# Performance work log

Hardware: AMD Instinct MI355X
Metric: run time of the kernel (lower is better)

Reference implementation:

```python
import jax, jax.numpy as jnp
import numpy as np

LEAKY_SLOPE = 0.01  # torch nn.LeakyReLU default
SOFTMAX_SCALE = 10.0
RATIO = 4


def _conv(x, w, b, stride, pad=1):
    y = jax.lax.conv_general_dilated(
        x, w, window_strides=(stride, stride), padding=[(pad, pad), (pad, pad)],
        dimension_numbers=("NCHW", "OIHW", "NCHW"))
    return y + b[None, :, None, None]


def _lrelu(x):
    return jnp.where(x >= 0, x, LEAKY_SLOPE * x)


def setup_inputs() -> dict:
    key = jax.random.key(0)
    ks = jax.random.split(key, 11)
    band_ms, band_hs = 8, 128
    inp = {
        "hrms": jax.random.normal(ks[0], (2, band_ms, 512, 512), jnp.float32),
        "msi": jax.random.normal(ks[1], (2, band_ms, 512, 512), jnp.float32),
        "hsi": jax.random.normal(ks[2], (2, band_hs, 128, 128), jnp.float32),
        "Wv": jax.random.normal(ks[3], (band_ms, band_ms, 3, 3), jnp.float32) * 0.05,
        "bv": jax.random.normal(ks[4], (band_ms,), jnp.float32) * 0.05,
        "Wq": jax.random.normal(ks[5], (band_ms, band_ms, 3, 3), jnp.float32) * 0.05,
        "bq": jax.random.normal(ks[6], (band_ms,), jnp.float32) * 0.05,
        "Wk": jax.random.normal(ks[7], (band_hs, band_hs, 3, 3), jnp.float32) * 0.05,
        "bk": jax.random.normal(ks[8], (band_hs,), jnp.float32) * 0.05,
        "Wr": jax.random.normal(ks[9], (band_hs, band_hs, 3, 3), jnp.float32) * 0.05,
        "br": jax.random.normal(ks[10], (band_hs,), jnp.float32) * 0.05,
    }
    return inp


def reference(hrms, msi, hsi, Wv, bv, Wq, bq, Wk, bk, Wr, br):
    # conv_v: 3x3 stride 1; conv_q: 3x3 stride ratio**2; conv_k: 3x3 stride ratio
    v = _lrelu(_conv(hrms, Wv, bv, 1))                 # (N, band_ms, H, W)
    q = _lrelu(_conv(msi, Wq, bq, RATIO * RATIO))      # (N, band_ms, 32, 32)
    k = _lrelu(_conv(hsi, Wk, bk, RATIO))              # (N, band_hs, 32, 32)

    # per-sample scalar normalization: max over bands of ||q_band||_2
    k0_max = jnp.max(jnp.sqrt(jnp.sum(q * q, axis=(2, 3))), axis=1)  # (N,)
    qn = q / k0_max[:, None, None, None]

    # Conv_spe with full-extent filter and stride == filter size reduces to a
    # global cross-spectral correlation: att[n, i, c] = <k[n,c], qn[n,i]>
    att = jnp.einsum("nihw,nchw->nic", qn, k)          # (N, band_ms, band_hs)
    att = jax.nn.softmax(att * SOFTMAX_SCALE, axis=2)  # softmax over band_hs

    # conv_transpose2d with 1x1 kernel (band_ms, band_hs, 1, 1) = pointwise mix
    out = jnp.einsum("nihw,nic->nchw", v, att) / 6.0   # (N, band_hs, H, W)
    return _lrelu(_conv(out, Wr, br, 1))
```

## Files before the change

### kernel.cpp

```cpp
#include <hip/hip_runtime.h>
#include <hip/hip_bf16.h>

#define LK 0.01f
__device__ __forceinline__ float lrelu(float x){ return x >= 0.f ? x : LK * x; }

#define NB 2
#define CMS 8
#define CHS 128
#define HW 512
#define HSIN 128
#define OS 32
#define K72 72

#define OFF_V   0
#define SZ_V    (NB*CMS*HW*HW)
#define OFF_Q   (OFF_V + SZ_V)
#define SZ_Q    (NB*CMS*OS*OS)
#define OFF_K   (OFF_Q + SZ_Q)
#define SZ_K    (NB*CHS*OS*OS)
#define OFF_BN  (OFF_K + SZ_K)
#define OFF_AR  (OFF_BN + 64)
#define SZ_AR   (NB*CMS*CHS)
#define OFF_A2  (OFF_AR + SZ_AR)
#define OFF_WE  (OFF_A2 + SZ_AR)
#define SZ_WE   (NB*K72*CHS)
#define OFF_WKT (OFF_WE + SZ_WE)
#define SZ_WKT  (1152*CHS)
#define OFF_WVT (OFF_WKT + SZ_WKT)
#define SZ_WVT  (K72*CMS)

__global__ void prep_kernel(const float* __restrict__ Wk, const float* __restrict__ Wv,
                            float* __restrict__ wkt, float* __restrict__ wvT){
  int idx = blockIdx.x * 256 + threadIdx.x;
  if (idx < 147456){
    int co = idx & 127, kk = idx >> 7;
    wkt[kk*128 + co] = Wk[co*1152 + kk];
  } else if (idx < 147456 + 576){
    int l = idx - 147456;
    int co = l & 7, kt = l >> 3;
    wvT[kt*8 + co] = Wv[co*72 + kt];
  }
}

__global__ __launch_bounds__(256, 4)
void conv_v_kernel(const float* __restrict__ hrms, const float* __restrict__ wvT,
                   const float* __restrict__ bv, float* __restrict__ v){
  __shared__ float vt[CMS][34][36];
  __shared__ __align__(16) float wl[K72*CMS];
  __shared__ float bvs[CMS];
  int xt = blockIdx.x, yt = blockIdx.y, n = blockIdx.z;
  int tid = threadIdx.x;
  for (int l = tid; l < CMS*34*34; l += 256){
    int ci = l / 1156, r = l % 1156, yy = r / 34, xx = r % 34;
    int gy = yt*32 + yy - 1, gx = xt*32 + xx - 1;
    float val = 0.f;
    if ((unsigned)gy < HW && (unsigned)gx < HW)
      val = hrms[((n*CMS+ci)*HW + gy)*HW + gx];
    vt[ci][yy][xx] = val;
  }
  for (int l = tid; l < K72*CMS; l += 256) wl[l] = wvT[l];
  if (tid < CMS) bvs[tid] = bv[tid];
  __syncthreads();
  int wid = tid >> 6;
  int lane = tid & 63;
  int lrow = lane >> 5, lx = lane & 31;
  for (int s = wid; s < 16; s += 4){
    int r0 = s*2 + lrow;
    float acc[8];
    #pragma unroll
    for (int c = 0; c < 8; c++) acc[c] = 0.f;
    #pragma unroll
    for (int ci = 0; ci < 8; ci++){
      float vv[9];
      #pragma unroll
      for (int t = 0; t < 9; t++) vv[t] = vt[ci][r0 + t/3][lx + t%3];
      #pragma unroll
      for (int tap = 0; tap < 9; tap++){
        const float4* wp = (const float4*)&wl[(ci*9 + tap)*8];
        float4 w0 = wp[0], w1 = wp[1];
        float vvt = vv[tap];
        acc[0] += w0.x*vvt; acc[1] += w0.y*vvt; acc[2] += w0.z*vvt; acc[3] += w0.w*vvt;
        acc[4] += w1.x*vvt; acc[5] += w1.y*vvt; acc[6] += w1.z*vvt; acc[7] += w1.w*vvt;
      }
    }
    int gy = yt*32 + r0, gx = xt*32 + lx;
    #pragma unroll
    for (int c = 0; c < 8; c++)
      v[((n*CMS+c)*HW + gy)*HW + gx] = lrelu(acc[c] + bvs[c]);
  }
}

__global__ void conv_q_kernel(const float* __restrict__ msi, const float* __restrict__ Wq,
                              const float* __restrict__ bq, float* __restrict__ q){
  __shared__ float rows[CMS][3][512];
  __shared__ float wq[K72*CMS];
  __shared__ float bqs[CMS];
  int n = blockIdx.x >> 5, y = blockIdx.x & 31;
  int tid = threadIdx.x;
  int y0 = y*16 - 1;
  for (int l = tid; l < CMS*3*512; l += 256){
    int ci = l / 1536, r = l % 1536, rr = r >> 9, xx = r & 511;
    int gy = y0 + rr;
    float val = 0.f;
    if ((unsigned)gy < HW) val = msi[((n*CMS+ci)*HW + gy)*HW + xx];
    rows[ci][rr][xx] = val;
  }
  for (int l = tid; l < K72*CMS; l += 256) wq[l] = Wq[l];
  if (tid < CMS) bqs[tid] = bq[tid];
  __syncthreads();
  int x = tid & 31, co = tid >> 5;
  int x0 = x*16 - 1;
  float acc = bqs[co];
  #pragma unroll
  for (int ci = 0; ci < 8; ci++){
    #pragma unroll
    for (int tap = 0; tap < 9; tap++){
      int xi = x0 + tap%3;
      float vv = ((unsigned)xi < HW) ? rows[ci][tap/3][xi] : 0.f;
      acc += vv * wq[co*72 + ci*9 + tap];
    }
  }
  q[((n*CMS+co)*OS + y)*OS + x] = lrelu(acc);
}

__global__ void bandnorm_kernel(const float* __restrict__ q, float* __restrict__ bn){
  int b = blockIdx.x;
  int tid = threadIdx.x;
  const float* qb = q + b*1024;
  float s = 0.f;
  for (int j = tid; j < 1024; j += 256){ float v = qb[j]; s += v*v; }
  __shared__ float red[4];
  for (int off = 32; off; off >>= 1) s += __shfl_down(s, off);
  if ((tid & 63) == 0) red[tid >> 6] = s;
  __syncthreads();
  if (tid == 0) bn[b] = sqrtf(red[0] + red[1] + red[2] + red[3]);
}

__global__ void conv_k_kernel(const float* __restrict__ hsi, const float* __restrict__ wkt,
                              const float* __restrict__ bk, float* __restrict__ kw){
  __shared__ __align__(16) float patch[1152][4];
  int xg = blockIdx.x, y = blockIdx.y, n = blockIdx.z;
  int tid = threadIdx.x;
  for (int l = tid; l < 4608; l += 128){
    int kk = l >> 2, xi = l & 3;
    int ci = kk / 9, tap = kk % 9;
    int gy = 4*y + tap/3 - 1, gx = 4*(xg*4 + xi) + tap%3 - 1;
    float val = 0.f;
    if ((unsigned)gy < HSIN && (unsigned)gx < HSIN)
      val = hsi[((n*CHS+ci)*HSIN + gy)*HSIN + gx];
    patch[kk][xi] = val;
  }
  __syncthreads();
  int co = tid;
  float bkv = bk[co];
  float a0 = bkv, a1 = bkv, a2 = bkv, a3 = bkv;
  #pragma unroll 8
  for (int kk = 0; kk < 1152; kk++){
    float4 p = *(const float4*)patch[kk];
    float w = wkt[kk*128 + co];
    a0 += p.x * w; a1 += p.y * w; a2 += p.z * w; a3 += p.w * w;
  }
  int base = ((n*CHS + co)*OS + y)*OS + xg*4;
  kw[base + 0] = lrelu(a0); kw[base + 1] = lrelu(a1);
  kw[base + 2] = lrelu(a2); kw[base + 3] = lrelu(a3);
}

__global__ void att_kernel(const float* __restrict__ q, const float* __restrict__ kw,
                           const float* __restrict__ bn, float* __restrict__ ar){
  int n = blockIdx.x >> 7, c = blockIdx.x & 127;
  int tid = threadIdx.x;
  const float* kb = kw + (n*CHS + c)*1024;
  float kreg[8];
  #pragma unroll
  for (int u = 0; u < 8; u++) kreg[u] = kb[tid + u*128];
  float m = bn[n*8];
  #pragma unroll
  for (int i = 1; i < 8; i++) m = fmaxf(m, bn[n*8 + i]);
  __shared__ float red[2];
  for (int i = 0; i < 8; i++){
    const float* qb = q + (n*CMS + i)*1024;
    float s = 0.f;
    #pragma unroll
    for (int u = 0; u < 8; u++) s += qb[tid + u*128] * kreg[u];
    for (int off = 32; off; off >>= 1) s += __shfl_down(s, off);
    if ((tid & 63) == 0) red[tid >> 6] = s;
    __syncthreads();
    if (tid == 0) ar[(n*CMS + i)*CHS + c] = (red[0] + red[1]) / m;
    __syncthreads();
  }
}

__global__ void softmax_kernel(const float* __restrict__ ar, float* __restrict__ a2){
  int b = blockIdx.x;
  int tid = threadIdx.x;
  float x = ar[b*128 + tid] * 10.f;
  __shared__ float red[2];
  float m = x;
  for (int off = 32; off; off >>= 1) m = fmaxf(m, __shfl_xor(m, off));
  if ((tid & 63) == 0) red[tid >> 6] = m;
  __syncthreads();
  m = fmaxf(red[0], red[1]);
  float e = expf(x - m);
  float s = e;
  for (int off = 32; off; off >>= 1) s += __shfl_xor(s, off);
  __syncthreads();
  if ((tid & 63) == 0) red[tid >> 6] = s;
  __syncthreads();
  s = red[0] + red[1];
  a2[b*128 + tid] = e / (6.f * s);
}

__global__ void weff_kernel(const float* __restrict__ Wr, const float* __restrict__ a2,
                            float* __restrict__ weT){
  int o = blockIdx.x & 127, n = blockIdx.x >> 7;
  int t = threadIdx.x;
  if (t >= 72) return;
  int i = t / 9, tap = t % 9;
  const float* av = a2 + (n*CMS + i)*CHS;
  float s = 0.f;
  for (int c = 0; c < 128; c++)
    s += Wr[(o*128 + c)*9 + tap] * av[c];
  weT[(n*K72 + t)*CHS + o] = s;
}

__global__ __launch_bounds__(512, 1)
void final_kernel(const float* __restrict__ v, const float* __restrict__ weT,
                  const float* __restrict__ br, float* __restrict__ out){
  __shared__ float vt[CMS][6][520];
  __shared__ __align__(16) float wl[K72*CHS];
  __shared__ float brs[CHS];
  int band = blockIdx.x, n = blockIdx.y;
  int tid = threadIdx.x;
  int r0 = band*4;
  for (int l = tid; l < CMS*6*512; l += 512){
    int i = l / 3072, rem = l - i*3072, r = rem >> 9, x = rem & 511;
    int gy = r0 - 1 + r;
    float val = 0.f;
    if ((unsigned)gy < HW) val = v[((n*CMS+i)*HW + gy)*HW + x];
    vt[i][r][x+1] = val;
  }
  if (tid < CMS*6){ int i = tid/6, r = tid - i*6; vt[i][r][0] = 0.f; vt[i][r][513] = 0.f; }
  for (int l = tid; l < K72*CHS; l += 512) wl[l] = weT[n*K72*CHS + l];
  if (tid < CHS) brs[tid] = br[tid];
  __syncthreads();
  int wid = __builtin_amdgcn_readfirstlane(tid >> 6);
  int lane = tid & 63;
  int ob = wid * 16;
  for (int cp = 0; cp < 4; cp++){
    int colA = cp*128 + lane;
    int colB = colA + 64;
    float accA[4][16], accB[4][16];
    #pragma unroll
    for (int rr = 0; rr < 4; rr++)
      #pragma unroll
      for (int j = 0; j < 16; j++){ accA[rr][j] = 0.f; accB[rr][j] = 0.f; }
    for (int i = 0; i < 8; i++){
      float vA[6][3], vB[6][3];
      #pragma unroll
      for (int r = 0; r < 6; r++){
        #pragma unroll
        for (int dc = 0; dc < 3; dc++){
          vA[r][dc] = vt[i][r][colA + dc];
          vB[r][dc] = vt[i][r][colB + dc];
        }
      }
      #pragma unroll
      for (int dy = 0; dy < 3; dy++){
        #pragma unroll
        for (int dx = 0; dx < 3; dx++){
          const float4* wp = (const float4*)&wl[(i*9 + dy*3 + dx)*CHS + ob];
          float4 w0 = wp[0], w1 = wp[1], w2 = wp[2], w3 = wp[3];
          #pragma unroll
          for (int rr = 0; rr < 4; rr++){
            float va = vA[rr + dy][dx];
            accA[rr][0]  += w0.x*va; accA[rr][1]  += w0.y*va; accA[rr][2]  += w0.z*va; accA[rr][3]  += w0.w*va;
            accA[rr][4]  += w1.x*va; accA[rr][5]  += w1.y*va; accA[rr][6]  += w1.z*va; accA[rr][7]  += w1.w*va;
            accA[rr][8]  += w2.x*va; accA[rr][9]  += w2.y*va; accA[rr][10] += w2.z*va; accA[rr][11] += w2.w*va;
            accA[rr][12] += w3.x*va; accA[rr][13] += w3.y*va; accA[rr][14] += w3.z*va; accA[rr][15] += w3.w*va;
            float vb = vB[rr + dy][dx];
            accB[rr][0]  += w0.x*vb; accB[rr][1]  += w0.y*vb; accB[rr][2]  += w0.z*vb; accB[rr][3]  += w0.w*vb;
            accB[rr][4]  += w1.x*vb; accB[rr][5]  += w1.y*vb; accB[rr][6]  += w1.z*vb; accB[rr][7]  += w1.w*vb;
            accB[rr][8]  += w2.x*vb; accB[rr][9]  += w2.y*vb; accB[rr][10] += w2.z*vb; accB[rr][11] += w2.w*vb;
            accB[rr][12] += w3.x*vb; accB[rr][13] += w3.y*vb; accB[rr][14] += w3.z*vb; accB[rr][15] += w3.w*vb;
          }
        }
      }
    }
    #pragma unroll
    for (int j = 0; j < 16; j++){
      int o = ob + j;
      float bb = brs[o];
      #pragma unroll
      for (int rr = 0; rr < 4; rr++){
        int rowbase = ((n*CHS + o)*HW + (r0 + rr))*HW;
        out[rowbase + colA] = lrelu(accA[rr][j] + bb);
        out[rowbase + colB] = lrelu(accB[rr][j] + bb);
      }
    }
  }
}

extern "C" void kernel_launch(void* const* d_in, const int* in_sizes, int n_in,
                              void* d_out, int out_size, void* d_ws, size_t ws_size,
                              hipStream_t stream){
  const float* hrms = (const float*)d_in[0];
  const float* msi  = (const float*)d_in[1];
  const float* hsi  = (const float*)d_in[2];
  const float* Wv   = (const float*)d_in[3];
  const float* bv   = (const float*)d_in[4];
  const float* Wq   = (const float*)d_in[5];
  const float* bq   = (const float*)d_in[6];
  const float* Wk   = (const float*)d_in[7];
  const float* bk   = (const float*)d_in[8];
  const float* Wr   = (const float*)d_in[9];
  const float* br   = (const float*)d_in[10];
  float* ws = (float*)d_ws;
  float* out = (float*)d_out;

  float* v   = ws + OFF_V;
  float* q   = ws + OFF_Q;
  float* kw  = ws + OFF_K;
  float* bn  = ws + OFF_BN;
  float* ar  = ws + OFF_AR;
  float* a2  = ws + OFF_A2;
  float* weT = ws + OFF_WE;
  float* wkt = ws + OFF_WKT;
  float* wvT = ws + OFF_WVT;

  hipLaunchKernelGGL(prep_kernel, dim3(579), dim3(256), 0, stream, Wk, Wv, wkt, wvT);
  hipLaunchKernelGGL(conv_v_kernel, dim3(16,16,2), dim3(256), 0, stream, hrms, wvT, bv, v);
  hipLaunchKernelGGL(conv_q_kernel, dim3(64), dim3(256), 0, stream, msi, Wq, bq, q);
  hipLaunchKernelGGL(bandnorm_kernel, dim3(16), dim3(256), 0, stream, q, bn);
  hipLaunchKernelGGL(conv_k_kernel, dim3(8,32,2), dim3(128), 0, stream, hsi, wkt, bk, kw);
  hipLaunchKernelGGL(att_kernel, dim3(256), dim3(128), 0, stream, q, kw, bn, ar);
  hipLaunchKernelGGL(softmax_kernel, dim3(16), dim3(128), 0, stream, ar, a2);
  hipLaunchKernelGGL(weff_kernel, dim3(256), dim3(128), 0, stream, Wr, a2, weT);
  hipLaunchKernelGGL(final_kernel, dim3(128, 2), dim3(512), 0, stream, v, weT, br, out);
}
```

Baseline: 591.0 us.

## Fuse conv_v into final kernel and tile-transpose Wk in prep

Removes the standalone conv_v kernel and its full-resolution v intermediate. The final kernel now computes the 3x3 stride-1 conv plus LeakyReLU on hrms for its 6-row band (with halo) directly into shared memory, prefetching each input channel into registers while computing the previous one. This avoids writing and re-reading about 16 MB of v to global memory, at the cost of recomputing halo rows (6 computed per 4 output rows), extra shared memory and register pressure in a kernel that runs only 256 blocks. The Wk transpose in prep now goes through a 64x64 shared-memory tile so both reads and writes are coalesced.

```diff
diff --git a/kernel.cpp b/kernel.cpp
--- a/kernel.cpp
+++ b/kernel.cpp
@@ -31,62 +31,21 @@
 
 __global__ void prep_kernel(const float* __restrict__ Wk, const float* __restrict__ Wv,
                             float* __restrict__ wkt, float* __restrict__ wvT){
-  int idx = blockIdx.x * 256 + threadIdx.x;
-  if (idx < 147456){
-    int co = idx & 127, kk = idx >> 7;
-    wkt[kk*128 + co] = Wk[co*1152 + kk];
-  } else if (idx < 147456 + 576){
-    int l = idx - 147456;
-    int co = l & 7, kt = l >> 3;
-    wvT[kt*8 + co] = Wv[co*72 + kt];
-  }
-}
-
-__global__ __launch_bounds__(256, 4)
-void conv_v_kernel(const float* __restrict__ hrms, const float* __restrict__ wvT,
-                   const float* __restrict__ bv, float* __restrict__ v){
-  __shared__ float vt[CMS][34][36];
-  __shared__ __align__(16) float wl[K72*CMS];
-  __shared__ float bvs[CMS];
-  int xt = blockIdx.x, yt = blockIdx.y, n = blockIdx.z;
-  int tid = threadIdx.x;
-  for (int l = tid; l < CMS*34*34; l += 256){
-    int ci = l / 1156, r = l % 1156, yy = r / 34, xx = r % 34;
-    int gy = yt*32 + yy - 1, gx = xt*32 + xx - 1;
-    float val = 0.f;
-    if ((unsigned)gy < HW && (unsigned)gx < HW)
-      val = hrms[((n*CMS+ci)*HW + gy)*HW + gx];
-    vt[ci][yy][xx] = val;
-  }
-  for (int l = tid; l < K72*CMS; l += 256) wl[l] = wvT[l];
-  if (tid < CMS) bvs[tid] = bv[tid];
-  __syncthreads();
-  int wid = tid >> 6;
-  int lane = tid & 63;
-  int lrow = lane >> 5, lx = lane & 31;
-  for (int s = wid; s < 16; s += 4){
-    int r0 = s*2 + lrow;
-    float acc[8];
-    #pragma unroll
-    for (int c = 0; c < 8; c++) acc[c] = 0.f;
-    #pragma unroll
-    for (int ci = 0; ci < 8; ci++){
-      float vv[9];
-      #pragma unroll
-      for (int t = 0; t < 9; t++) vv[t] = vt[ci][r0 + t/3][lx + t%3];
-      #pragma unroll
-      for (int tap = 0; tap < 9; tap++){
-        const float4* wp = (const float4*)&wl[(ci*9 + tap)*8];
-        float4 w0 = wp[0], w1 = wp[1];
-        float vvt = vv[tap];
-        acc[0] += w0.x*vvt; acc[1] += w0.y*vvt; acc[2] += w0.z*vvt; acc[3] += w0.w*vvt;
-        acc[4] += w1.x*vvt; acc[5] += w1.y*vvt; acc[6] += w1.z*vvt; acc[7] += w1.w*vvt;
-      }
-    }
-    int gy = yt*32 + r0, gx = xt*32 + lx;
-    #pragma unroll
-    for (int c = 0; c < 8; c++)
-      v[((n*CMS+c)*HW + gy)*HW + gx] = lrelu(acc[c] + bvs[c]);
+  __shared__ float t[64][65];
+  int bx = blockIdx.x, by = blockIdx.y;
+  int tx = threadIdx.x & 63, ty = threadIdx.x >> 6;
+  #pragma unroll
+  for (int r = ty; r < 64; r += 4)
+    t[r][tx] = Wk[(by*64 + r)*1152 + bx*64 + tx];
+  __syncthreads();
+  #pragma unroll
+  for (int r = ty; r < 64; r += 4)
+    wkt[(bx*64 + r)*128 + by*64 + tx] = t[tx][r];
+  if (bx == 0 && by == 0){
+    for (int l = threadIdx.x; l < 576; l += 256){
+      int co = l & 7, kt = l >> 3;
+      wvT[kt*8 + co] = Wv[co*72 + kt];
+    }
   }
 }
 
@@ -224,25 +183,93 @@
 }
 
 __global__ __launch_bounds__(512, 1)
-void final_kernel(const float* __restrict__ v, const float* __restrict__ weT,
+void final_kernel(const float* __restrict__ hrms, const float* __restrict__ wvT,
+                  const float* __restrict__ bv, const float* __restrict__ weT,
                   const float* __restrict__ br, float* __restrict__ out){
   __shared__ float vt[CMS][6][520];
   __shared__ __align__(16) float wl[K72*CHS];
+  __shared__ float hbuf[8][520];
+  __shared__ __align__(16) float wvs[K72*CMS];
   __shared__ float brs[CHS];
+  __shared__ float bvs[CMS];
   int band = blockIdx.x, n = blockIdx.y;
   int tid = threadIdx.x;
   int r0 = band*4;
-  for (int l = tid; l < CMS*6*512; l += 512){
-    int i = l / 3072, rem = l - i*3072, r = rem >> 9, x = rem & 511;
+  for (int l = tid; l < K72*CHS; l += 512) wl[l] = weT[n*K72*CHS + l];
+  for (int l = tid; l < K72*CMS; l += 512) wvs[l] = wvT[l];
+  if (tid < CHS) brs[tid] = br[tid];
+  if (tid < CMS) bvs[tid] = bv[tid];
+  if (tid < CMS*6){ int i = tid/6, r = tid - i*6; vt[i][r][0] = 0.f; vt[i][r][513] = 0.f; }
+
+  int col = tid;
+  float acc_v[6][8];
+  #pragma unroll
+  for (int r = 0; r < 6; r++)
+    #pragma unroll
+    for (int c = 0; c < 8; c++) acc_v[r][c] = 0.f;
+
+  float stg[9];
+  {
+    const float* hp = hrms + (size_t)(n*CMS + 0)*HW*HW;
+    #pragma unroll
+    for (int u = 0; u < 9; u++){
+      int l = tid + u*512;
+      float val = 0.f;
+      if (l < 4112){
+        int row = l / 514, cc = l - row*514;
+        int gy = r0 - 2 + row, gx = cc - 1;
+        if ((unsigned)gy < HW && (unsigned)gx < HW) val = hp[gy*HW + gx];
+      }
+      stg[u] = val;
+    }
+  }
+  for (int ci = 0; ci < 8; ci++){
+    __syncthreads();
+    #pragma unroll
+    for (int u = 0; u < 9; u++){
+      int l = tid + u*512;
+      if (l < 4112){ int row = l / 514, cc = l - row*514; hbuf[row][cc] = stg[u]; }
+    }
+    __syncthreads();
+    if (ci < 7){
+      const float* hp = hrms + (size_t)(n*CMS + ci + 1)*HW*HW;
+      #pragma unroll
+      for (int u = 0; u < 9; u++){
+        int l = tid + u*512;
+        float val = 0.f;
+        if (l < 4112){
+          int row = l / 514, cc = l - row*514;
+          int gy = r0 - 2 + row, gx = cc - 1;
+          if ((unsigned)gy < HW && (unsigned)gx < HW) val = hp[gy*HW + gx];
+        }
+        stg[u] = val;
+      }
+    }
+    #pragma unroll
+    for (int tap = 0; tap < 9; tap++){
+      const float4* wp = (const float4*)&wvs[(ci*9 + tap)*8];
+      float4 w0 = wp[0], w1 = wp[1];
+      int dy = tap/3, dx = tap%3;
+      #pragma unroll
+      for (int r = 0; r < 6; r++){
+        float hb = hbuf[r + dy][col + dx];
+        acc_v[r][0] += w0.x*hb; acc_v[r][1] += w0.y*hb; acc_v[r][2] += w0.z*hb; acc_v[r][3] += w0.w*hb;
+        acc_v[r][4] += w1.x*hb; acc_v[r][5] += w1.y*hb; acc_v[r][6] += w1.z*hb; acc_v[r][7] += w1.w*hb;
+      }
+    }
+  }
+  #pragma unroll
+  for (int r = 0; r < 6; r++){
     int gy = r0 - 1 + r;
-    float val = 0.f;
-    if ((unsigned)gy < HW) val = v[((n*CMS+i)*HW + gy)*HW + x];
-    vt[i][r][x+1] = val;
-  }
-  if (tid < CMS*6){ int i = tid/6, r = tid - i*6; vt[i][r][0] = 0.f; vt[i][r][513] = 0.f; }
-  for (int l = tid; l < K72*CHS; l += 512) wl[l] = weT[n*K72*CHS + l];
-  if (tid < CHS) brs[tid] = br[tid];
-  __syncthreads();
+    bool ok = (unsigned)gy < HW;
+    #pragma unroll
+    for (int c = 0; c < 8; c++){
+      float t = acc_v[r][c] + bvs[c];
+      vt[c][r][col + 1] = ok ? (t >= 0.f ? t : LK*t) : 0.f;
+    }
+  }
+  __syncthreads();
+
   int wid = __builtin_amdgcn_readfirstlane(tid >> 6);
   int lane = tid & 63;
   int ob = wid * 16;
@@ -317,7 +344,6 @@
   float* ws = (float*)d_ws;
   float* out = (float*)d_out;
 
-  float* v   = ws + OFF_V;
   float* q   = ws + OFF_Q;
   float* kw  = ws + OFF_K;
   float* bn  = ws + OFF_BN;
@@ -327,13 +353,13 @@
   float* wkt = ws + OFF_WKT;
   float* wvT = ws + OFF_WVT;
 
-  hipLaunchKernelGGL(prep_kernel, dim3(579), dim3(256), 0, stream, Wk, Wv, wkt, wvT);
-  hipLaunchKernelGGL(conv_v_kernel, dim3(16,16,2), dim3(256), 0, stream, hrms, wvT, bv, v);
+  hipLaunchKernelGGL(prep_kernel, dim3(18, 2), dim3(256), 0, stream, Wk, Wv, wkt, wvT);
   hipLaunchKernelGGL(conv_q_kernel, dim3(64), dim3(256), 0, stream, msi, Wq, bq, q);
   hipLaunchKernelGGL(bandnorm_kernel, dim3(16), dim3(256), 0, stream, q, bn);
   hipLaunchKernelGGL(conv_k_kernel, dim3(8,32,2), dim3(128), 0, stream, hsi, wkt, bk, kw);
   hipLaunchKernelGGL(att_kernel, dim3(256), dim3(128), 0, stream, q, kw, bn, ar);
   hipLaunchKernelGGL(softmax_kernel, dim3(16), dim3(128), 0, stream, ar, a2);
   hipLaunchKernelGGL(weff_kernel, dim3(256), dim3(128), 0, stream, Wr, a2, weT);
-  hipLaunchKernelGGL(final_kernel, dim3(128, 2), dim3(512), 0, stream, v, weT, br, out);
-}
+  hipLaunchKernelGGL(final_kernel, dim3(128, 2), dim3(512), 0, stream,
+                     hrms, wvT, bv, weT, br, out);
+}
```

After: 522.1 us. 1.13x faster.
